# Kernel tuning notes

Measured on AMD Instinct MI355X. Metric: run time of the kernel, lower is better.

## Reference

```python
import jax, jax.numpy as jnp
import numpy as np

N, E, D_IN, H, L, C = 50000, 800000, 500, 256, 4, 7
ALPHA, GAMMA, EPS = 0.5, 0.5, 0.1  # self-loop weight, parallel-edge weight, FAConv eps
LN_EPS = 1e-5


def setup_inputs() -> dict:
    key = jax.random.key(0)
    ks = jax.random.split(key, 8)
    x = jax.random.normal(ks[0], (N, D_IN), jnp.float32)
    src = jax.random.randint(ks[1], (E,), 0, N, jnp.int32)
    dst = jax.random.randint(ks[2], (E,), 0, N, jnp.int32)
    dst = jnp.where(dst == src, (dst + 1) % N, dst)  # ensure no self-loops (remove_self_loops is then a no-op)
    edge_index = jnp.stack([src, dst])
    s_in = 1.0 / np.sqrt(D_IN)
    s_h = 1.0 / np.sqrt(H)
    W_init = jax.random.uniform(ks[3], (H, D_IN), jnp.float32, -s_in, s_in)
    b_init = jnp.zeros((H,), jnp.float32)
    att_l = jax.random.uniform(ks[4], (L, H), jnp.float32, -s_h, s_h)
    att_r = jax.random.uniform(ks[5], (L, H), jnp.float32, -s_h, s_h)
    ln_g = jnp.ones((L, H), jnp.float32)
    ln_b = jnp.zeros((L, H), jnp.float32)
    W_last = jax.random.uniform(ks[6], (C, H), jnp.float32, -s_h, s_h)
    b_last = jnp.zeros((C,), jnp.float32)
    return dict(x=x, edge_index=edge_index, W_init=W_init, b_init=b_init,
                att_l=att_l, att_r=att_r, ln_g=ln_g, ln_b=ln_b,
                W_last=W_last, b_last=b_last)


def _layernorm(x, g, b):
    mu = jnp.mean(x, axis=-1, keepdims=True)
    var = jnp.var(x, axis=-1, keepdims=True)
    return (x - mu) * jax.lax.rsqrt(var + LN_EPS) * g + b


def reference(x, edge_index, W_init, b_init, att_l, att_r, ln_g, ln_b, W_last, b_last):
    num_nodes = x.shape[0]
    num_edges = edge_index.shape[1]
    x = x @ W_init.T + b_init  # [N, H]
    x0 = x
    # add self-loops after parallel edges
    loop = jnp.arange(num_nodes, dtype=edge_index.dtype)
    src = jnp.concatenate([edge_index[0], loop])
    dst = jnp.concatenate([edge_index[1], loop])
    ew = jnp.concatenate([jnp.full((num_edges,), GAMMA, x.dtype),
                          jnp.full((num_nodes,), ALPHA, x.dtype)])
    for i in range(L):
        # FAConv: alpha_e = tanh(att_l.x_src + att_r.x_dst); msg = x_src * alpha_e * ew
        al = x @ att_l[i]  # [N]
        ar = x @ att_r[i]  # [N]
        a_e = jnp.tanh(al[src] + ar[dst]) * ew  # [E+N]
        msg = x[src] * a_e[:, None]            # [E+N, H]
        agg = jax.ops.segment_sum(msg, dst, num_segments=num_nodes)
        x = agg + EPS * x0
        if i != L - 1:
            x = _layernorm(jax.nn.relu(x), ln_g[i], ln_b[i])
            # F.dropout with p=0.0 is identity
    emb = x @ W_last.T + b_last  # [N, C]
    return emb, jax.nn.log_softmax(emb, axis=1)
```

## Files before the change

### kernel.cpp

```cpp
#include <hip/hip_runtime.h>
#include <hip/hip_fp16.h>

#define N_NODES 50000
#define N_EDGES 800000
#define D_IN_K  500
#define K_PAD   512
#define H_DIM   256
#define N_CLS   7
#define ALPHA_W 0.5f
#define GAMMA_W 0.5f
#define EPS_W   0.1f
#define LN_EPS_W 1e-5f

#define SCAN_B 256
#define SCAN_NB ((N_NODES + SCAN_B - 1) / SCAN_B)

typedef unsigned short u16;
typedef unsigned int   u32;
typedef _Float16 f16;
typedef __attribute__((ext_vector_type(8))) _Float16 f16x8;
typedef __attribute__((ext_vector_type(4))) float    f32x4;
typedef __attribute__((ext_vector_type(8))) unsigned short u16x8;

__device__ __forceinline__ float h2f(u16 v) {
    __half h;
    *reinterpret_cast<u16*>(&h) = v;
    return __half2float(h);
}
__device__ __forceinline__ u16 f2h(float f) {
    __half h = __float2half_rn(f);
    return *reinterpret_cast<u16*>(&h);
}
__device__ __forceinline__ int clampN(int v) {
    return (v < 0) ? 0 : ((v >= N_NODES) ? N_NODES - 1 : v);
}

__global__ __launch_bounds__(256) void sentinel_kernel(float* out, int n) {
    int i = blockIdx.x * blockDim.x + threadIdx.x;
    if (i < n) out[i] = 2.0f;
}

__global__ __launch_bounds__(256) void zero_kernel(int* p, int n) {
    int i = blockIdx.x * blockDim.x + threadIdx.x;
    if (i < n) p[i] = 0;
}

__global__ __launch_bounds__(256) void hist_kernel(const int* __restrict__ dst, int* __restrict__ deg, int e) {
    int i = blockIdx.x * blockDim.x + threadIdx.x;
    if (i < e) atomicAdd(&deg[clampN(dst[i])], 1);
}

__global__ __launch_bounds__(SCAN_B) void scan_a(const int* __restrict__ deg, int* __restrict__ row_ptr,
                                                 int* __restrict__ bsum) {
    __shared__ int sdata[SCAN_B];
    int t = threadIdx.x;
    int i = blockIdx.x * SCAN_B + t;
    int v = (i < N_NODES) ? deg[i] : 0;
    sdata[t] = v;
    __syncthreads();
#pragma unroll
    for (int off = 1; off < SCAN_B; off <<= 1) {
        int a = (t >= off) ? sdata[t - off] : 0;
        __syncthreads();
        sdata[t] += a;
        __syncthreads();
    }
    if (i < N_NODES) row_ptr[i] = sdata[t] - v;
    if (t == SCAN_B - 1) bsum[blockIdx.x] = sdata[t];
}

__global__ __launch_bounds__(SCAN_B) void scan_b(int* __restrict__ bsum, int* __restrict__ boff,
                                                 int* __restrict__ row_ptr) {
    __shared__ int sdata[SCAN_B];
    int t = threadIdx.x;
    int v = (t < SCAN_NB) ? bsum[t] : 0;
    sdata[t] = v;
    __syncthreads();
#pragma unroll
    for (int off = 1; off < SCAN_B; off <<= 1) {
        int a = (t >= off) ? sdata[t - off] : 0;
        __syncthreads();
        sdata[t] += a;
        __syncthreads();
    }
    if (t < SCAN_NB) boff[t] = sdata[t] - v;
    if (t == SCAN_B - 1) row_ptr[N_NODES] = sdata[t];
}

__global__ __launch_bounds__(SCAN_B) void scan_c(int* __restrict__ row_ptr, const int* __restrict__ boff) {
    int i = blockIdx.x * SCAN_B + threadIdx.x;
    if (i < N_NODES) row_ptr[i] += boff[blockIdx.x];
}

__global__ __launch_bounds__(256) void scatter_kernel(const int* __restrict__ src, const int* __restrict__ dst,
                                                      const int* __restrict__ row_ptr, int* __restrict__ deg,
                                                      int* __restrict__ srcS, int e) {
    int i = blockIdx.x * blockDim.x + threadIdx.x;
    if (i < e) {
        int d = clampN(dst[i]);
        int old = atomicSub(&deg[d], 1);
        int pos = row_ptr[d] + old - 1;
        if (pos >= 0 && pos < e) srcS[pos] = clampN(src[i]);
    }
}

__global__ __launch_bounds__(256) void convert_w(const float* __restrict__ W, f16* __restrict__ W16) {
    int i = blockIdx.x * 256 + threadIdx.x;
    int n = i >> 9, k = i & (K_PAD - 1);
    W16[i] = (k < D_IN_K) ? (f16)W[n * D_IN_K + k] : (f16)0.f;
}

#define W_STRIDE 520
__global__ __launch_bounds__(256) void mfma_gemm3(const float* __restrict__ X,
                                                  const f16* __restrict__ W16,
                                                  const float* __restrict__ bias,
                                                  u16* __restrict__ out) {
    __shared__ __align__(16) f16 wlds[32 * W_STRIDE];
    int tid  = threadIdx.x;
    int wl   = tid >> 6;
    int lane = tid & 63;
    int m    = lane & 15;
    int quad = lane >> 4;

    int node = blockIdx.x * 64 + wl * 16 + m;
    int nodec = (node < N_NODES) ? node : N_NODES - 1;

    f16x8 a[16];
    const float* ap = X + (long)nodec * D_IN_K;
#pragma unroll
    for (int kc = 0; kc < 16; kc++) {
        int kbase = kc * 32 + quad * 8;
        f16x8 av;
        if (kbase + 8 <= D_IN_K) {
            float4 lo = *(const float4*)(ap + kbase);
            float4 hi = *(const float4*)(ap + kbase + 4);
            av[0] = (f16)lo.x; av[1] = (f16)lo.y; av[2] = (f16)lo.z; av[3] = (f16)lo.w;
            av[4] = (f16)hi.x; av[5] = (f16)hi.y; av[6] = (f16)hi.z; av[7] = (f16)hi.w;
        } else {
#pragma unroll
            for (int t = 0; t < 8; t++)
                av[t] = (kbase + t < D_IN_K) ? (f16)ap[kbase + t] : (f16)0.f;
        }
        a[kc] = av;
    }

    for (int p = 0; p < 8; p++) {
        __syncthreads();
        for (int idx = tid; idx < 32 * 64; idx += 256) {
            int row = idx >> 6, c = idx & 63;
            *(f16x8*)&wlds[row * W_STRIDE + c * 8] = *(const f16x8*)&W16[((p << 5) + row) * K_PAD + c * 8];
        }
        __syncthreads();

        f32x4 acc[2];
#pragma unroll
        for (int t = 0; t < 2; t++) acc[t] = (f32x4){0.f, 0.f, 0.f, 0.f};

        for (int kc = 0; kc < 16; kc++) {
#pragma unroll
            for (int t = 0; t < 2; t++) {
                f16x8 b = *(const f16x8*)&wlds[(t * 16 + m) * W_STRIDE + kc * 32 + quad * 8];
                acc[t] = __builtin_amdgcn_mfma_f32_16x16x32_f16(a[kc], b, acc[t], 0, 0, 0);
            }
        }

        int nb = blockIdx.x * 64 + wl * 16 + quad * 4;
#pragma unroll
        for (int t = 0; t < 2; t++) {
            int h = (p << 5) + t * 16 + m;
            float bv = bias[h];
#pragma unroll
            for (int r = 0; r < 4; r++) {
                int nrow = nb + r;
                if (nrow < N_NODES) out[(long)nrow * H_DIM + h] = f2h(acc[t][r] + bv);
            }
        }
    }
}

__global__ __launch_bounds__(256) void alar_kernel(const u16* __restrict__ x,
                                                   const float* __restrict__ attl,
                                                   const float* __restrict__ attr,
                                                   float* __restrict__ al, float* __restrict__ ar, int n) {
    int w = (blockIdx.x * blockDim.x + threadIdx.x) >> 6;
    int lane = threadIdx.x & 63;
    if (w >= n) return;
    int col = lane * 4;
    ushort4 xv = *(const ushort4*)(x + (long)w * H_DIM + col);
    float4 lv = *(const float4*)(attl + col);
    float4 rv = *(const float4*)(attr + col);
    float x0 = h2f(xv.x), x1 = h2f(xv.y), x2 = h2f(xv.z), x3 = h2f(xv.w);
    float pl = x0 * lv.x + x1 * lv.y + x2 * lv.z + x3 * lv.w;
    float pr = x0 * rv.x + x1 * rv.y + x2 * rv.z + x3 * rv.w;
#pragma unroll
    for (int off = 32; off >= 1; off >>= 1) {
        pl += __shfl_xor(pl, off);
        pr += __shfl_xor(pr, off);
    }
    if (lane == 0) { al[w] = pl; ar[w] = pr; }
}

__global__ __launch_bounds__(256) void layer_kernel3(const u16* __restrict__ xin,
                                                     const u16* __restrict__ x0,
                                                     const float* __restrict__ alIn,
                                                     float* __restrict__ alOut,
                                                     float* __restrict__ ar,
                                                     const int* __restrict__ row_ptr,
                                                     const int* __restrict__ srcS,
                                                     const float* __restrict__ g,
                                                     const float* __restrict__ b,
                                                     const float* __restrict__ attlN,
                                                     const float* __restrict__ attrN,
                                                     u16* __restrict__ xout,
                                                     const float* __restrict__ Wl,
                                                     const float* __restrict__ bl,
                                                     float* __restrict__ outF,
                                                     int n, int mode) {
    int w = (blockIdx.x * blockDim.x + threadIdx.x) >> 6;
    int lane = threadIdx.x & 63;
    if (w >= n) return;
    int half = lane >> 5;
    int sub  = lane & 31;
    int col  = sub * 8;

    float arn = ar[w];
    float aself = ALPHA_W * tanhf(alIn[w] + arn);

    float acc[8];
    if (half == 0) {
        u16x8 xs  = *(const u16x8*)(xin + (long)w * H_DIM + col);
        u16x8 x0v = *(const u16x8*)(x0  + (long)w * H_DIM + col);
#pragma unroll
        for (int k = 0; k < 8; k++) acc[k] = aself * h2f(xs[k]) + EPS_W * h2f(x0v[k]);
    } else {
#pragma unroll
        for (int k = 0; k < 8; k++) acc[k] = 0.f;
    }

    int e0 = row_ptr[w], e1 = row_ptr[w + 1];
    for (int base = e0; base < e1; base += 64) {
        int cnt = e1 - base; if (cnt > 64) cnt = 64;
        int s = 0; float a = 0.f;
        if (lane < cnt) {
            s = clampN(srcS[base + lane]);
            a = GAMMA_W * tanhf(alIn[s] + arn);
        }
        for (int j = 0; j < cnt; j += 8) {
            int i0 = j + half, i1 = j + 2 + half, i2 = j + 4 + half, i3 = j + 6 + half;
            int s0 = __shfl(s, i0), s1 = __shfl(s, i1), s2 = __shfl(s, i2), s3 = __shfl(s, i3);
            float c0 = __shfl(a, i0), c1 = __shfl(a, i1), c2 = __shfl(a, i2), c3 = __shfl(a, i3);
            u16x8 v0 = *(const u16x8*)(xin + (long)s0 * H_DIM + col);
            u16x8 v1 = *(const u16x8*)(xin + (long)s1 * H_DIM + col);
            u16x8 v2 = *(const u16x8*)(xin + (long)s2 * H_DIM + col);
            u16x8 v3 = *(const u16x8*)(xin + (long)s3 * H_DIM + col);
#pragma unroll
            for (int k = 0; k < 8; k++) {
                acc[k] = fmaf(c0, h2f(v0[k]), acc[k]);
                acc[k] = fmaf(c1, h2f(v1[k]), acc[k]);
                acc[k] = fmaf(c2, h2f(v2[k]), acc[k]);
                acc[k] = fmaf(c3, h2f(v3[k]), acc[k]);
            }
        }
    }

#pragma unroll
    for (int k = 0; k < 8; k++) acc[k] += __shfl(acc[k], lane ^ 32);

    if (mode == 0) {
        float v[8];
        float sum = 0.f, sq = 0.f;
#pragma unroll
        for (int k = 0; k < 8; k++) {
            v[k] = fmaxf(acc[k], 0.f);
            sum += v[k];
            sq  += v[k] * v[k];
        }
#pragma unroll
        for (int off = 16; off >= 1; off >>= 1) {
            sum += __shfl_xor(sum, off);
            sq  += __shfl_xor(sq, off);
        }
        float mu = sum * (1.f / 256.f);
        float var = fmaxf(sq * (1.f / 256.f) - mu * mu, 0.f);
        float rstd = rsqrtf(var + LN_EPS_W);
        float4 ga = *(const float4*)(g + col);
        float4 gb = *(const float4*)(g + col + 4);
        float4 ba = *(const float4*)(b + col);
        float4 bb = *(const float4*)(b + col + 4);
        float gg[8]  = {ga.x, ga.y, ga.z, ga.w, gb.x, gb.y, gb.z, gb.w};
        float bbv[8] = {ba.x, ba.y, ba.z, ba.w, bb.x, bb.y, bb.z, bb.w};
        float4 la = *(const float4*)(attlN + col);
        float4 lb = *(const float4*)(attlN + col + 4);
        float4 ra = *(const float4*)(attrN + col);
        float4 rb = *(const float4*)(attrN + col + 4);
        float ll[8] = {la.x, la.y, la.z, la.w, lb.x, lb.y, lb.z, lb.w};
        float rr[8] = {ra.x, ra.y, ra.z, ra.w, rb.x, rb.y, rb.z, rb.w};
        float pl = 0.f, pr = 0.f;
        u16x8 o;
#pragma unroll
        for (int k = 0; k < 8; k++) {
            float val = (v[k] - mu) * rstd * gg[k] + bbv[k];
            o[k] = f2h(val);
            pl += val * ll[k];
            pr += val * rr[k];
        }
#pragma unroll
        for (int off = 16; off >= 1; off >>= 1) {
            pl += __shfl_xor(pl, off);
            pr += __shfl_xor(pr, off);
        }
        if (lane == 0) { alOut[w] = pl; ar[w] = pr; }
        if (half == 0) *(u16x8*)(xout + (long)w * H_DIM + col) = o;
    } else {
        float p[N_CLS];
#pragma unroll
        for (int c = 0; c < N_CLS; c++) {
            const float* wr = Wl + c * H_DIM + col;
            float4 wa = *(const float4*)(wr);
            float4 wb = *(const float4*)(wr + 4);
            p[c] = acc[0] * wa.x + acc[1] * wa.y + acc[2] * wa.z + acc[3] * wa.w
                 + acc[4] * wb.x + acc[5] * wb.y + acc[6] * wb.z + acc[7] * wb.w;
        }
#pragma unroll
        for (int off = 16; off >= 1; off >>= 1) {
#pragma unroll
            for (int c = 0; c < N_CLS; c++) p[c] += __shfl_xor(p[c], off);
        }
        if (lane == 0) {
            float e[N_CLS];
            float m = -1e30f;
#pragma unroll
            for (int c = 0; c < N_CLS; c++) {
                e[c] = p[c] + bl[c];
                m = fmaxf(m, e[c]);
            }
            float sx = 0.f;
#pragma unroll
            for (int c = 0; c < N_CLS; c++) sx += expf(e[c] - m);
            float lse = logf(sx);
#pragma unroll
            for (int c = 0; c < N_CLS; c++) {
                outF[(long)w * N_CLS + c] = e[c];
                outF[(long)N_NODES * N_CLS + (long)w * N_CLS + c] = e[c] - m - lse;
            }
        }
    }
}

extern "C" void kernel_launch(void* const* d_in, const int* in_sizes, int n_in,
                              void* d_out, int out_size, void* d_ws, size_t ws_size,
                              hipStream_t stream) {
    const float* x_in   = (const float*)d_in[0];
    const int*   ei     = (const int*)d_in[1];
    const float* W_init = (const float*)d_in[2];
    const float* b_init = (const float*)d_in[3];
    const float* att_l  = (const float*)d_in[4];
    const float* att_r  = (const float*)d_in[5];
    const float* ln_g   = (const float*)d_in[6];
    const float* ln_b   = (const float*)d_in[7];
    const float* W_last = (const float*)d_in[8];
    const float* b_last = (const float*)d_in[9];
    float* out = (float*)d_out;

    const size_t OFF_X0  = 0;
    const size_t OFF_XA  = 25600000;
    const size_t OFF_XB  = 51200000;
    const size_t OFF_AL  = 76800000;
    const size_t OFF_AR  = 77000000;
    const size_t OFF_DEG = 77200000;
    const size_t OFF_RP  = 77400000;
    const size_t OFF_SRC = 77600064;
    const size_t OFF_BS  = 80800064;
    const size_t OFF_BO  = 80801088;
    const size_t WS_NEED = 80802112;

    if (ws_size < WS_NEED) {
        sentinel_kernel<<<(out_size + 255) / 256, 256, 0, stream>>>(out, out_size);
        return;
    }

    char* ws = (char*)d_ws;
    u16* x0  = (u16*)(ws + OFF_X0);
    u16* xA  = (u16*)(ws + OFF_XA);
    u16* xB  = (u16*)(ws + OFF_XB);
    f16* W16 = (f16*)(ws + OFF_AL);
    float* al  = (float*)(ws + OFF_AL);
    float* ar  = (float*)(ws + OFF_AR);
    float* al2 = (float*)(ws + OFF_DEG);
    int* deg     = (int*)(ws + OFF_DEG);
    int* row_ptr = (int*)(ws + OFF_RP);
    int* srcS    = (int*)(ws + OFF_SRC);
    int* bsum    = (int*)(ws + OFF_BS);
    int* boff    = (int*)(ws + OFF_BO);

    const int* e_src = ei;
    const int* e_dst = ei + N_EDGES;

    int zb = (N_NODES + 255) / 256;
    zero_kernel<<<zb, 256, 0, stream>>>(deg, N_NODES);
    int eb = (N_EDGES + 255) / 256;
    hist_kernel<<<eb, 256, 0, stream>>>(e_dst, deg, N_EDGES);
    scan_a<<<SCAN_NB, SCAN_B, 0, stream>>>(deg, row_ptr, bsum);
    scan_b<<<1, SCAN_B, 0, stream>>>(bsum, boff, row_ptr);
    scan_c<<<SCAN_NB, SCAN_B, 0, stream>>>(row_ptr, boff);
    scatter_kernel<<<eb, 256, 0, stream>>>(e_src, e_dst, row_ptr, deg, srcS, N_EDGES);

    convert_w<<<(H_DIM * K_PAD) / 256, 256, 0, stream>>>(W_init, W16);
    mfma_gemm3<<<(N_NODES + 63) / 64, 256, 0, stream>>>(x_in, W16, b_init, x0);

    int nb = (N_NODES * 64 + 255) / 256;
    alar_kernel<<<nb, 256, 0, stream>>>(x0, att_l, att_r, al, ar, N_NODES);

    const u16* bufs_in[4]   = {x0, xA, xB, xA};
    u16* bufs_out[4]        = {xA, xB, xA, xB};
    const float* al_in[4]   = {al, al2, al, al2};
    float* al_out[4]        = {al2, al, al2, al};
    for (int i = 0; i < 4; i++) {
        int nxt = (i < 3) ? (i + 1) : i;
        layer_kernel3<<<nb, 256, 0, stream>>>(bufs_in[i], x0, al_in[i], al_out[i], ar,
                                              row_ptr, srcS,
                                              ln_g + i * H_DIM, ln_b + i * H_DIM,
                                              att_l + nxt * H_DIM, att_r + nxt * H_DIM,
                                              bufs_out[i], W_last, b_last, out,
                                              N_NODES, (i < 3) ? 0 : 1);
    }
}
```

Measured before the change: 574.2 us.

## Make input GEMM persistent with register-resident weights and double-buffered row tiles

Replaces the per-64-node GEMM, which reloaded all of W into LDS eight times per block, with a persistent kernel of 256 blocks × 1024 threads. Each of the 16 waves keeps a 16-column slice of W in registers. The blocks stride over 16-node tiles of X, converting each tile to fp16 and double-buffering it through LDS so the next tile's global load overlaps the current MFMAs. This removes repeated weight traffic and per-block setup. The cost is one 16x256 output tile per iteration, a barrier on every tile, and no tail handling, which relies on N being divisible by 16.

```diff
diff --git a/kernel.cpp b/kernel.cpp
--- a/kernel.cpp
+++ b/kernel.cpp
@@ -110,71 +110,83 @@
     W16[i] = (k < D_IN_K) ? (f16)W[n * D_IN_K + k] : (f16)0.f;
 }
 
-#define W_STRIDE 520
-__global__ __launch_bounds__(256) void mfma_gemm3(const float* __restrict__ X,
-                                                  const f16* __restrict__ W16,
-                                                  const float* __restrict__ bias,
-                                                  u16* __restrict__ out) {
-    __shared__ __align__(16) f16 wlds[32 * W_STRIDE];
+#define GW_STRIDE 520
+#define GA_BUF    (16 * GW_STRIDE)
+
+__device__ __forceinline__ f16x8 stage_load(const float* __restrict__ X, int tile, int r, int sc) {
+    const float* p = X + (long)(tile * 16 + r) * D_IN_K + sc;
+    f16x8 v;
+    if (sc + 8 <= D_IN_K) {
+        float4 lo = *(const float4*)(p);
+        float4 hi = *(const float4*)(p + 4);
+        v[0] = (f16)lo.x; v[1] = (f16)lo.y; v[2] = (f16)lo.z; v[3] = (f16)lo.w;
+        v[4] = (f16)hi.x; v[5] = (f16)hi.y; v[6] = (f16)hi.z; v[7] = (f16)hi.w;
+    } else {
+#pragma unroll
+        for (int t = 0; t < 8; t++)
+            v[t] = (sc + t < D_IN_K) ? (f16)p[t] : (f16)0.f;
+    }
+    return v;
+}
+
+__global__ __launch_bounds__(1024) void mfma_gemm5(const float* __restrict__ X,
+                                                   const f16* __restrict__ W16,
+                                                   const float* __restrict__ bias,
+                                                   u16* __restrict__ out) {
+    __shared__ __align__(16) f16 alds[2 * GA_BUF];
+
     int tid  = threadIdx.x;
-    int wl   = tid >> 6;
+    int w    = tid >> 6;
     int lane = tid & 63;
     int m    = lane & 15;
     int quad = lane >> 4;
-
-    int node = blockIdx.x * 64 + wl * 16 + m;
-    int nodec = (node < N_NODES) ? node : N_NODES - 1;
-
-    f16x8 a[16];
-    const float* ap = X + (long)nodec * D_IN_K;
-#pragma unroll
-    for (int kc = 0; kc < 16; kc++) {
-        int kbase = kc * 32 + quad * 8;
-        f16x8 av;
-        if (kbase + 8 <= D_IN_K) {
-            float4 lo = *(const float4*)(ap + kbase);
-            float4 hi = *(const float4*)(ap + kbase + 4);
-            av[0] = (f16)lo.x; av[1] = (f16)lo.y; av[2] = (f16)lo.z; av[3] = (f16)lo.w;
-            av[4] = (f16)hi.x; av[5] = (f16)hi.y; av[6] = (f16)hi.z; av[7] = (f16)hi.w;
-        } else {
-#pragma unroll
-            for (int t = 0; t < 8; t++)
-                av[t] = (kbase + t < D_IN_K) ? (f16)ap[kbase + t] : (f16)0.f;
-        }
-        a[kc] = av;
-    }
-
-    for (int p = 0; p < 8; p++) {
+    int h    = w * 16 + m;
+
+    f16x8 bfrag[16];
+    {
+        const f16* wb = W16 + (long)h * K_PAD + quad * 8;
+#pragma unroll
+        for (int kc = 0; kc < 16; kc++)
+            bfrag[kc] = *(const f16x8*)(wb + kc * 32);
+    }
+    float bv = bias[h];
+
+    int sr = w;
+    int sc = lane * 8;
+
+    int nt = N_NODES / 16;
+    int t  = blockIdx.x;
+    int buf = 0;
+
+    if (t < nt) {
+        f16x8 sv = stage_load(X, t, sr, sc);
+        *(f16x8*)&alds[sr * GW_STRIDE + sc] = sv;
+    }
+    __syncthreads();
+
+    while (t < nt) {
+        int tn = t + (int)gridDim.x;
+        bool hn = (tn < nt);
+        f16x8 nsv;
+        if (hn) nsv = stage_load(X, tn, sr, sc);
+
+        f32x4 acc = (f32x4){0.f, 0.f, 0.f, 0.f};
+        const f16* ab = &alds[buf * GA_BUF + m * GW_STRIDE + quad * 8];
+#pragma unroll
+        for (int kc = 0; kc < 16; kc++) {
+            f16x8 a = *(const f16x8*)(ab + kc * 32);
+            acc = __builtin_amdgcn_mfma_f32_16x16x32_f16(a, bfrag[kc], acc, 0, 0, 0);
+        }
+
+        long nb = (long)t * 16 + quad * 4;
+#pragma unroll
+        for (int r = 0; r < 4; r++)
+            out[(nb + r) * H_DIM + h] = f2h(acc[r] + bv);
+
+        if (hn) *(f16x8*)&alds[(buf ^ 1) * GA_BUF + sr * GW_STRIDE + sc] = nsv;
         __syncthreads();
-        for (int idx = tid; idx < 32 * 64; idx += 256) {
-            int row = idx >> 6, c = idx & 63;
-            *(f16x8*)&wlds[row * W_STRIDE + c * 8] = *(const f16x8*)&W16[((p << 5) + row) * K_PAD + c * 8];
-        }
-        __syncthreads();
-
-        f32x4 acc[2];
-#pragma unroll
-        for (int t = 0; t < 2; t++) acc[t] = (f32x4){0.f, 0.f, 0.f, 0.f};
-
-        for (int kc = 0; kc < 16; kc++) {
-#pragma unroll
-            for (int t = 0; t < 2; t++) {
-                f16x8 b = *(const f16x8*)&wlds[(t * 16 + m) * W_STRIDE + kc * 32 + quad * 8];
-                acc[t] = __builtin_amdgcn_mfma_f32_16x16x32_f16(a[kc], b, acc[t], 0, 0, 0);
-            }
-        }
-
-        int nb = blockIdx.x * 64 + wl * 16 + quad * 4;
-#pragma unroll
-        for (int t = 0; t < 2; t++) {
-            int h = (p << 5) + t * 16 + m;
-            float bv = bias[h];
-#pragma unroll
-            for (int r = 0; r < 4; r++) {
-                int nrow = nb + r;
-                if (nrow < N_NODES) out[(long)nrow * H_DIM + h] = f2h(acc[t][r] + bv);
-            }
-        }
+        buf ^= 1;
+        t = tn;
     }
 }
 
@@ -406,7 +418,7 @@
     scatter_kernel<<<eb, 256, 0, stream>>>(e_src, e_dst, row_ptr, deg, srcS, N_EDGES);
 
     convert_w<<<(H_DIM * K_PAD) / 256, 256, 0, stream>>>(W_init, W16);
-    mfma_gemm3<<<(N_NODES + 63) / 64, 256, 0, stream>>>(x_in, W16, b_init, x0);
+    mfma_gemm5<<<256, 1024, 0, stream>>>(x_in, W16, b_init, x0);
 
     int nb = (N_NODES * 64 + 255) / 256;
     alar_kernel<<<nb, 256, 0, stream>>>(x0, att_l, att_r, al, ar, N_NODES);
```

Result: faster. 548.7 us (-4.4%).
